# Performance work log

Measured on AMD Instinct MI355X. Metric: run time of the kernel, lower is better.

## Reference

```python
import jax, jax.numpy as jnp
import numpy as np

W0_SIREN = 30.0  # omega_0 used in sine activations

HID = [64, 64, 256, 256, 256]
IN_DIM = 65   # 64 feat channels + 1 time channel
OUT_DIM = 64


def _siren_params(key):
    dims = [IN_DIM] + HID + [OUT_DIM]
    params = []
    for i in range(len(dims) - 1):
        fan_in, fan_out = dims[i], dims[i + 1]
        key, kw, kb = jax.random.split(key, 3)
        if i == 0:
            bound = 1.0 / fan_in
        else:
            bound = np.sqrt(6.0 / fan_in) / W0_SIREN
        W = jax.random.uniform(kw, (fan_out, fan_in), jnp.float32, -bound, bound)
        b = jax.random.uniform(kb, (fan_out,), jnp.float32, -bound, bound)
        params.append((W, b))
    return params


def setup_inputs() -> dict:
    key = jax.random.key(0)
    k_feat, k_t, k_p = jax.random.split(key, 3)
    feat = jax.random.normal(k_feat, (2, 64, 192, 320), jnp.float32)
    times = jax.random.uniform(k_t, (3,), jnp.float32)
    params = _siren_params(k_p)
    inp = {"feat": feat, "times": times}
    for i, (W, b) in enumerate(params):
        inp[f"w{i}"] = W
        inp[f"b{i}"] = b
    return inp


def _gather_full_grid(feat):
    """Nearest grid_sample (align_corners=False) at pixel-center coords over the full grid.
    Returns [B, H*W, C]."""
    B, C, H, W = feat.shape
    # make_coord pixel centers in [-1, 1]
    ys = -1.0 + (2.0 * jnp.arange(H, dtype=jnp.float32) + 1.0) / H
    xs = -1.0 + (2.0 * jnp.arange(W, dtype=jnp.float32) + 1.0) / W
    gy, gx = jnp.meshgrid(ys, xs, indexing="ij")          # [H, W] each
    gy, gx = gy.reshape(-1), gx.reshape(-1)               # [qs]
    # grid_sample nearest, align_corners=False unnormalization
    iy = jnp.clip(jnp.round(((gy + 1.0) * H - 1.0) / 2.0).astype(jnp.int32), 0, H - 1)
    ix = jnp.clip(jnp.round(((gx + 1.0) * W - 1.0) / 2.0).astype(jnp.int32), 0, W - 1)
    q = feat[:, :, iy, ix]                                # [B, C, qs] gather
    return jnp.transpose(q, (0, 2, 1))                    # [B, qs, C]


def _siren_mlp(x, ws, bs):
    h = x
    n = len(ws)
    for i in range(n - 1):
        h = jnp.sin(W0_SIREN * (h @ ws[i].T + bs[i]))
    return h @ ws[n - 1].T + bs[n - 1]                    # outermost linear


def reference(feat, times, w0, b0, w1, b1, w2, b2, w3, b3, w4, b4, w5, b5):
    ws = [w0, w1, w2, w3, w4, w5]
    bs = [b0, b1, b2, b3, b4, b5]
    B, C, H, W = feat.shape
    qs = H * W
    q_feat = _gather_full_grid(feat)                      # [B, qs, 64]
    preds = []
    for c in range(3):  # Training==True branch: 3 time stamps
        t = times[c]
        pe = jnp.full((B, qs, 1), 1.0, feat.dtype) * t    # time channel
        enc = jnp.concatenate([q_feat, pe], axis=-1)      # [B, qs, 65]
        out = _siren_mlp(enc.reshape(B * qs, IN_DIM), ws, bs)  # [B*qs, 64]
        # F.fold with kernel_size=1 == reshape back to spatial map
        pred = out.reshape(B, qs, OUT_DIM).transpose(0, 2, 1).reshape(B, OUT_DIM, H, W)
        preds.append(pred)
    return jnp.stack(preds, axis=0)                       # [3, B, 64, H, W]
```

## Files before the change

### kernel.cpp

```cpp
#include <hip/hip_runtime.h>
#include <hip/hip_bf16.h>

typedef __bf16 bf16_t;
typedef bf16_t bf16x8 __attribute__((ext_vector_type(8)));
typedef float f32x4 __attribute__((ext_vector_type(4)));
typedef unsigned short u16;
typedef unsigned int u32;

static constexpr int kHW = 192 * 320;
static constexpr float kC = 4.77464829275686f;

__device__ __forceinline__ u16 f2bf(float f) {
  u32 u = __float_as_uint(f);
  return (u16)((u + 0x7FFFu + ((u >> 16) & 1u)) >> 16);
}

__device__ __forceinline__ u32 pack2(float a, float b) {
  __hip_bfloat162 h = __float22bfloat162_rn(make_float2(a, b));
  union { __hip_bfloat162 h2; u32 u; } cv;
  cv.h2 = h;
  return cv.u;
}

__device__ __forceinline__ void lds_barrier() {
  __asm__ volatile("s_waitcnt lgkmcnt(0)\n\ts_barrier" ::: "memory");
}

static constexpr int OFF_W0 = 0;
static constexpr int OFF_W1 = 4096;
static constexpr int OFF_W2 = 8192;
static constexpr int OFF_W3 = 24576;
static constexpr int OFF_W4 = 90112;
static constexpr int OFF_W5 = 155648;
static constexpr int W_TOTAL = 172032;
static constexpr int B_TOTAL = 1024;
static constexpr size_t FEAT_BYTE_OFF = 348160;
static constexpr size_t WS_NEED = FEAT_BYTE_OFF + (size_t)1920 * 8192;

__global__ void convert_weights(const float* __restrict__ w0, const float* __restrict__ w1,
                                const float* __restrict__ w2, const float* __restrict__ w3,
                                const float* __restrict__ w4, const float* __restrict__ w5,
                                const float* __restrict__ b0, const float* __restrict__ b1,
                                const float* __restrict__ b2, const float* __restrict__ b3,
                                const float* __restrict__ b4, const float* __restrict__ b5,
                                u16* __restrict__ wb, float* __restrict__ bws) {
  int i = blockIdx.x * 256 + threadIdx.x;
  if (i < W_TOTAL) {
    float v, s = kC;
    if (i < OFF_W1)      { int o = i >> 6, k = i & 63; v = w0[o * 65 + k]; }
    else if (i < OFF_W2) { v = w1[i - OFF_W1]; }
    else if (i < OFF_W3) { v = w2[i - OFF_W2]; }
    else if (i < OFF_W4) { v = w3[i - OFF_W3]; }
    else if (i < OFF_W5) { v = w4[i - OFF_W4]; }
    else                 { v = w5[i - OFF_W5]; s = 1.0f; }
    wb[i] = f2bf(v * s);
  } else {
    int j = i - W_TOTAL;
    float v;
    if (j < 64)       v = kC * b0[j];
    else if (j < 128) v = kC * w0[(j - 64) * 65 + 64];
    else if (j < 192) v = kC * b1[j - 128];
    else if (j < 448) v = kC * b2[j - 192];
    else if (j < 704) v = kC * b3[j - 448];
    else if (j < 960) v = kC * b4[j - 704];
    else              v = b5[j - 960];
    bws[j] = v;
  }
}

__global__ void convert_feat(const float* __restrict__ feat, u16* __restrict__ featT) {
  const int chunk = blockIdx.x;
  const int bq  = chunk / 960;
  const int hw0 = (chunk % 960) * 64;
  const int tid = threadIdx.x;
  const int p   = tid & 63;
  const int gg  = tid >> 6;
  const float* fbase = feat + (size_t)bq * 64 * kHW + hw0 + p;
  u16* img = featT + (size_t)chunk * 4096;
#pragma unroll
  for (int j = 0; j < 2; ++j) {
    const int g = gg * 2 + j;
    float v[8];
#pragma unroll
    for (int e = 0; e < 8; ++e) v[e] = fbase[(size_t)(g * 8 + e) * kHW];
    uint4 pk;
    pk.x = pack2(v[0], v[1]);
    pk.y = pack2(v[2], v[3]);
    pk.z = pack2(v[4], v[5]);
    pk.w = pack2(v[6], v[7]);
    *reinterpret_cast<uint4*>(img + p * 64 + ((g ^ (p & 7)) * 8)) = pk;
  }
}

template<int RSO>
__device__ __forceinline__ void epilogue_sin(f32x4 acc, u16* outb, int p, int g,
                                             int quad, int sw) {
  float s0 = __builtin_amdgcn_sinf(__builtin_amdgcn_fractf(acc[0]));
  float s1 = __builtin_amdgcn_sinf(__builtin_amdgcn_fractf(acc[1]));
  float s2 = __builtin_amdgcn_sinf(__builtin_amdgcn_fractf(acc[2]));
  float s3 = __builtin_amdgcn_sinf(__builtin_amdgcn_fractf(acc[3]));
  uint2 v;
  v.x = pack2(s0, s1);
  v.y = pack2(s2, s3);
  *reinterpret_cast<uint2*>(outb + p * RSO + ((g ^ sw) * 8) + (quad & 1) * 4) = v;
}

template<int NOT, int KT, int K>
__device__ __forceinline__ void load_wf(bf16x8 (&wf)[NOT][KT], const u16* __restrict__ wb,
                                        int wave, int l15, int quad) {
#pragma unroll
  for (int ks = 0; ks < KT; ++ks)
#pragma unroll
    for (int ot = 0; ot < NOT; ++ot)
      wf[ot][ks] = *reinterpret_cast<const bf16x8*>(
          wb + ((wave * NOT + ot) * 16 + l15) * K + ks * 32 + quad * 8);
}

template<int NOT>
__device__ __forceinline__ void load_bv(f32x4 (&bv)[NOT], const float* __restrict__ bg,
                                        int wave, int quad) {
#pragma unroll
  for (int ot = 0; ot < NOT; ++ot)
    bv[ot] = *reinterpret_cast<const f32x4*>(bg + (wave * NOT + ot) * 16 + quad * 4);
}

template<bool PRE>
__global__ void __launch_bounds__(256, 2)
siren_main(const float* __restrict__ feat, const float* __restrict__ times,
           const u16* __restrict__ wb, const float* __restrict__ bws,
           const u16* __restrict__ featT, float* __restrict__ out) {
  __shared__ __align__(16) u16 A32[64 * 256];
  __shared__ __align__(16) u16 B32[64 * 256];
  u16* X = B32;
  u16* Y = B32 + 4096;

  const int tid   = threadIdx.x;
  const int bid   = blockIdx.x;
  const int c     = bid / 1920;
  const int chunk = bid % 1920;
  const int bq    = chunk / 960;
  const int hw0   = (chunk % 960) * 64;
  const float t   = times[c];
  const int wave  = tid >> 6;
  const int lane  = tid & 63;
  const int l15   = lane & 15;
  const int quad  = lane >> 4;
  const int sw    = l15 & 7;

  bf16x8 wf0[1][2], wf1[1][2];
  load_wf<1, 2, 64>(wf0, wb + OFF_W0, wave, l15, quad);
  load_wf<1, 2, 64>(wf1, wb + OFF_W1, wave, l15, quad);
  f32x4 bv0;
  {
    f32x4 cb = *reinterpret_cast<const f32x4*>(bws + wave * 16 + quad * 4);
    f32x4 cw = *reinterpret_cast<const f32x4*>(bws + 64 + wave * 16 + quad * 4);
#pragma unroll
    for (int r = 0; r < 4; ++r) bv0[r] = cb[r] + t * cw[r];
  }
  f32x4 bv1 = *reinterpret_cast<const f32x4*>(bws + 128 + wave * 16 + quad * 4);

  if constexpr (PRE) {
    const uint4* src = reinterpret_cast<const uint4*>(featT + (size_t)chunk * 4096);
    uint4* dst = reinterpret_cast<uint4*>(X);
    dst[tid]       = src[tid];
    dst[tid + 256] = src[tid + 256];
  } else {
    const int p  = tid & 63;
    const int gg = tid >> 6;
    const float* fbase = feat + (size_t)bq * 64 * kHW + hw0 + p;
#pragma unroll
    for (int j = 0; j < 2; ++j) {
      const int g = gg * 2 + j;
      float v[8];
#pragma unroll
      for (int e = 0; e < 8; ++e) v[e] = fbase[(size_t)(g * 8 + e) * kHW];
      uint4 pk;
      pk.x = pack2(v[0], v[1]);
      pk.y = pack2(v[2], v[3]);
      pk.z = pack2(v[4], v[5]);
      pk.w = pack2(v[6], v[7]);
      *reinterpret_cast<uint4*>(X + p * 64 + ((g ^ (p & 7)) * 8)) = pk;
    }
  }
  lds_barrier();

  bf16x8 wf2[4][2];
  f32x4  bv2[4];
  {
    bf16x8 af[4][2];
#pragma unroll
    for (int pt = 0; pt < 4; ++pt)
#pragma unroll
      for (int ks = 0; ks < 2; ++ks)
        af[pt][ks] = *reinterpret_cast<const bf16x8*>(
            X + (pt * 16 + l15) * 64 + (((ks * 4 + quad) ^ sw) * 8));
    f32x4 acc[4];
#pragma unroll
    for (int pt = 0; pt < 4; ++pt) {
      acc[pt] = bv0;
      acc[pt] = __builtin_amdgcn_mfma_f32_16x16x32_bf16(wf0[0][0], af[pt][0], acc[pt], 0, 0, 0);
      acc[pt] = __builtin_amdgcn_mfma_f32_16x16x32_bf16(wf0[0][1], af[pt][1], acc[pt], 0, 0, 0);
    }
    load_wf<4, 2, 64>(wf2, wb + OFF_W2, wave, l15, quad);
    load_bv<4>(bv2, bws + 192, wave, quad);
#pragma unroll
    for (int pt = 0; pt < 4; ++pt)
      epilogue_sin<64>(acc[pt], Y, pt * 16 + l15, wave * 2 + (quad >> 1), quad, sw);
  }
  lds_barrier();

  {
    bf16x8 af[4][2];
#pragma unroll
    for (int pt = 0; pt < 4; ++pt)
#pragma unroll
      for (int ks = 0; ks < 2; ++ks)
        af[pt][ks] = *reinterpret_cast<const bf16x8*>(
            Y + (pt * 16 + l15) * 64 + (((ks * 4 + quad) ^ sw) * 8));
    f32x4 acc[4];
#pragma unroll
    for (int pt = 0; pt < 4; ++pt) {
      acc[pt] = bv1;
      acc[pt] = __builtin_amdgcn_mfma_f32_16x16x32_bf16(wf1[0][0], af[pt][0], acc[pt], 0, 0, 0);
      acc[pt] = __builtin_amdgcn_mfma_f32_16x16x32_bf16(wf1[0][1], af[pt][1], acc[pt], 0, 0, 0);
    }
#pragma unroll
    for (int pt = 0; pt < 4; ++pt)
      epilogue_sin<64>(acc[pt], X, pt * 16 + l15, wave * 2 + (quad >> 1), quad, sw);
  }
  lds_barrier();

  bf16x8 wf3[4][8];
  f32x4  bv3[4];
  {
    bf16x8 af[4][2];
#pragma unroll
    for (int pt = 0; pt < 4; ++pt)
#pragma unroll
      for (int ks = 0; ks < 2; ++ks)
        af[pt][ks] = *reinterpret_cast<const bf16x8*>(
            X + (pt * 16 + l15) * 64 + (((ks * 4 + quad) ^ sw) * 8));
    f32x4 acc[4][4];
#pragma unroll
    for (int pt = 0; pt < 4; ++pt)
#pragma unroll
      for (int ot = 0; ot < 4; ++ot) {
        acc[pt][ot] = bv2[ot];
        acc[pt][ot] = __builtin_amdgcn_mfma_f32_16x16x32_bf16(wf2[ot][0], af[pt][0], acc[pt][ot], 0, 0, 0);
        acc[pt][ot] = __builtin_amdgcn_mfma_f32_16x16x32_bf16(wf2[ot][1], af[pt][1], acc[pt][ot], 0, 0, 0);
      }
    load_wf<4, 8, 256>(wf3, wb + OFF_W3, wave, l15, quad);
    load_bv<4>(bv3, bws + 448, wave, quad);
#pragma unroll
    for (int pt = 0; pt < 4; ++pt)
#pragma unroll
      for (int ot = 0; ot < 4; ++ot)
        epilogue_sin<256>(acc[pt][ot], A32, pt * 16 + l15,
                          (wave * 4 + ot) * 2 + (quad >> 1), quad, sw);
  }
  lds_barrier();

  bf16x8 wf4[4][8];
  f32x4  bv4[4];
  {
#pragma unroll
    for (int pt = 0; pt < 4; ++pt) {
      bf16x8 af[8];
#pragma unroll
      for (int ks = 0; ks < 8; ++ks)
        af[ks] = *reinterpret_cast<const bf16x8*>(
            A32 + (pt * 16 + l15) * 256 + (((ks * 4 + quad) ^ sw) * 8));
      f32x4 acc[4];
#pragma unroll
      for (int ot = 0; ot < 4; ++ot) acc[ot] = bv3[ot];
#pragma unroll
      for (int ks = 0; ks < 8; ++ks)
#pragma unroll
        for (int ot = 0; ot < 4; ++ot)
          acc[ot] = __builtin_amdgcn_mfma_f32_16x16x32_bf16(wf3[ot][ks], af[ks], acc[ot], 0, 0, 0);
      if (pt == 3) {
        load_wf<4, 8, 256>(wf4, wb + OFF_W4, wave, l15, quad);
        load_bv<4>(bv4, bws + 704, wave, quad);
      }
#pragma unroll
      for (int ot = 0; ot < 4; ++ot)
        epilogue_sin<256>(acc[ot], B32, pt * 16 + l15,
                          (wave * 4 + ot) * 2 + (quad >> 1), quad, sw);
    }
  }
  lds_barrier();

  bf16x8 wf5[1][8];
  f32x4  bv5;
  {
#pragma unroll
    for (int pt = 0; pt < 4; ++pt) {
      bf16x8 af[8];
#pragma unroll
      for (int ks = 0; ks < 8; ++ks)
        af[ks] = *reinterpret_cast<const bf16x8*>(
            B32 + (pt * 16 + l15) * 256 + (((ks * 4 + quad) ^ sw) * 8));
      f32x4 acc[4];
#pragma unroll
      for (int ot = 0; ot < 4; ++ot) acc[ot] = bv4[ot];
#pragma unroll
      for (int ks = 0; ks < 8; ++ks)
#pragma unroll
        for (int ot = 0; ot < 4; ++ot)
          acc[ot] = __builtin_amdgcn_mfma_f32_16x16x32_bf16(wf4[ot][ks], af[ks], acc[ot], 0, 0, 0);
      if (pt == 3) {
        load_wf<1, 8, 256>(wf5, wb + OFF_W5, wave, l15, quad);
        bv5 = *reinterpret_cast<const f32x4*>(bws + 960 + wave * 16 + quad * 4);
      }
#pragma unroll
      for (int ot = 0; ot < 4; ++ot)
        epilogue_sin<256>(acc[ot], A32, pt * 16 + l15,
                          (wave * 4 + ot) * 2 + (quad >> 1), quad, sw);
    }
  }
  lds_barrier();

  {
    float* out_base = out + (size_t)(c * 2 + bq) * 64 * kHW + hw0;
#pragma unroll
    for (int pt = 0; pt < 4; ++pt) {
      bf16x8 af[8];
#pragma unroll
      for (int ks = 0; ks < 8; ++ks)
        af[ks] = *reinterpret_cast<const bf16x8*>(
            A32 + (pt * 16 + l15) * 256 + (((ks * 4 + quad) ^ sw) * 8));
      f32x4 acc = bv5;
#pragma unroll
      for (int ks = 0; ks < 8; ++ks)
        acc = __builtin_amdgcn_mfma_f32_16x16x32_bf16(wf5[0][ks], af[ks], acc, 0, 0, 0);
      const int p = pt * 16 + l15;
      const int o = wave * 16 + quad * 4;
      float* dst = out_base + (size_t)o * kHW + p;
#pragma unroll
      for (int r = 0; r < 4; ++r) dst[(size_t)r * kHW] = acc[r];
    }
  }
}

extern "C" void kernel_launch(void* const* d_in, const int* in_sizes, int n_in,
                              void* d_out, int out_size, void* d_ws, size_t ws_size,
                              hipStream_t stream) {
  const float* feat  = (const float*)d_in[0];
  const float* times = (const float*)d_in[1];
  const float* w0 = (const float*)d_in[2];
  const float* b0 = (const float*)d_in[3];
  const float* w1 = (const float*)d_in[4];
  const float* b1 = (const float*)d_in[5];
  const float* w2 = (const float*)d_in[6];
  const float* b2 = (const float*)d_in[7];
  const float* w3 = (const float*)d_in[8];
  const float* b3 = (const float*)d_in[9];
  const float* w4 = (const float*)d_in[10];
  const float* b4 = (const float*)d_in[11];
  const float* w5 = (const float*)d_in[12];
  const float* b5 = (const float*)d_in[13];
  u16*   wb  = (u16*)d_ws;
  float* bws = (float*)((char*)d_ws + (size_t)W_TOTAL * 2);
  float* out = (float*)d_out;

  convert_weights<<<(W_TOTAL + B_TOTAL) / 256, 256, 0, stream>>>(
      w0, w1, w2, w3, w4, w5, b0, b1, b2, b3, b4, b5, wb, bws);

  if (ws_size >= WS_NEED) {
    u16* featT = (u16*)((char*)d_ws + FEAT_BYTE_OFF);
    convert_feat<<<1920, 256, 0, stream>>>(feat, featT);
    siren_main<true><<<5760, 256, 0, stream>>>(feat, times, wb, bws, featT, out);
  } else {
    siren_main<false><<<5760, 256, 0, stream>>>(feat, times, wb, bws, wb, out);
  }
}
```

Baseline: 393.0 us.

## Software-pipeline LDS operand reads and split weight prefetch across layers

Restructures every layer so the LDS operand fragments for the next point tile are read while the current tile's MFMAs and sine epilogue run, using two double-buffered fragment sets. Weight prefetch for the 256-wide layers is split into two halves issued at different points to spread register pressure and global-load latency. In the PRE path, layer 0 now reads its operands directly from the pre-transposed global buffer, skipping the LDS staging copy and one barrier. The trade-off is higher register pressure; occupancy is pinned with waves_per_eu(2,2), which risks spills.

```diff
diff --git a/kernel.cpp b/kernel.cpp
--- a/kernel.cpp
+++ b/kernel.cpp
@@ -105,27 +105,13 @@
   *reinterpret_cast<uint2*>(outb + p * RSO + ((g ^ sw) * 8) + (quad & 1) * 4) = v;
 }
 
-template<int NOT, int KT, int K>
-__device__ __forceinline__ void load_wf(bf16x8 (&wf)[NOT][KT], const u16* __restrict__ wb,
-                                        int wave, int l15, int quad) {
-#pragma unroll
-  for (int ks = 0; ks < KT; ++ks)
-#pragma unroll
-    for (int ot = 0; ot < NOT; ++ot)
-      wf[ot][ks] = *reinterpret_cast<const bf16x8*>(
-          wb + ((wave * NOT + ot) * 16 + l15) * K + ks * 32 + quad * 8);
-}
-
-template<int NOT>
-__device__ __forceinline__ void load_bv(f32x4 (&bv)[NOT], const float* __restrict__ bg,
-                                        int wave, int quad) {
-#pragma unroll
-  for (int ot = 0; ot < NOT; ++ot)
-    bv[ot] = *reinterpret_cast<const f32x4*>(bg + (wave * NOT + ot) * 16 + quad * 4);
+__device__ __forceinline__ f32x4 mf(bf16x8 a, bf16x8 b, f32x4 c) {
+  return __builtin_amdgcn_mfma_f32_16x16x32_bf16(a, b, c, 0, 0, 0);
 }
 
 template<bool PRE>
-__global__ void __launch_bounds__(256, 2)
+__global__ __attribute__((amdgpu_waves_per_eu(2, 2)))
+void __launch_bounds__(256)
 siren_main(const float* __restrict__ feat, const float* __restrict__ times,
            const u16* __restrict__ wb, const float* __restrict__ bws,
            const u16* __restrict__ featT, float* __restrict__ out) {
@@ -147,192 +133,289 @@
   const int quad  = lane >> 4;
   const int sw    = l15 & 7;
 
-  bf16x8 wf0[1][2], wf1[1][2];
-  load_wf<1, 2, 64>(wf0, wb + OFF_W0, wave, l15, quad);
-  load_wf<1, 2, 64>(wf1, wb + OFF_W1, wave, l15, quad);
-  f32x4 bv0;
+  auto read_af8 = [&](bf16x8 (&af)[8], const u16* in, int pt) {
+#pragma unroll
+    for (int ks = 0; ks < 8; ++ks)
+      af[ks] = *reinterpret_cast<const bf16x8*>(
+          in + (pt * 16 + l15) * 256 + (((ks * 4 + quad) ^ sw) * 8));
+  };
+  auto read_af2 = [&](bf16x8 (&af)[2], const u16* in, int pt) {
+#pragma unroll
+    for (int ks = 0; ks < 2; ++ks)
+      af[ks] = *reinterpret_cast<const bf16x8*>(
+          in + (pt * 16 + l15) * 64 + (((ks * 4 + quad) ^ sw) * 8));
+  };
+  auto load_wf_half = [&](bf16x8 (&wf)[4][4], const u16* wbase, int kh) {
+#pragma unroll
+    for (int ks = 0; ks < 4; ++ks)
+#pragma unroll
+      for (int ot = 0; ot < 4; ++ot)
+        wf[ot][ks] = *reinterpret_cast<const bf16x8*>(
+            wbase + ((wave * 4 + ot) * 16 + l15) * 256 + (kh * 4 + ks) * 32 + quad * 8);
+  };
+  auto load_bv4 = [&](f32x4 (&bv)[4], const float* bg) {
+#pragma unroll
+    for (int ot = 0; ot < 4; ++ot)
+      bv[ot] = *reinterpret_cast<const f32x4*>(bg + (wave * 4 + ot) * 16 + quad * 4);
+  };
+  auto mfma_pt = [&](f32x4 (&acc)[4], bf16x8 (&wa)[4][4], bf16x8 (&wbh)[4][4],
+                     bf16x8 (&af)[8], const f32x4 (&bv)[4]) {
+#pragma unroll
+    for (int ot = 0; ot < 4; ++ot) acc[ot] = bv[ot];
+#pragma unroll
+    for (int ks = 0; ks < 8; ++ks)
+#pragma unroll
+      for (int ot = 0; ot < 4; ++ot)
+        acc[ot] = mf(ks < 4 ? wa[ot][ks] : wbh[ot][ks - 4], af[ks], acc[ot]);
+  };
+  auto epi_pt4 = [&](f32x4 (&acc)[4], u16* outb, int pt) {
+#pragma unroll
+    for (int ot = 0; ot < 4; ++ot)
+      epilogue_sin<256>(acc[ot], outb, pt * 16 + l15,
+                        (wave * 4 + ot) * 2 + (quad >> 1), quad, sw);
+  };
+
+  bf16x8 wf0[2], wf1[2];
+#pragma unroll
+  for (int ks = 0; ks < 2; ++ks) {
+    wf0[ks] = *reinterpret_cast<const bf16x8*>(wb + OFF_W0 + (wave * 16 + l15) * 64 + ks * 32 + quad * 8);
+    wf1[ks] = *reinterpret_cast<const bf16x8*>(wb + OFF_W1 + (wave * 16 + l15) * 64 + ks * 32 + quad * 8);
+  }
+  f32x4 bv0, bv1;
   {
     f32x4 cb = *reinterpret_cast<const f32x4*>(bws + wave * 16 + quad * 4);
     f32x4 cw = *reinterpret_cast<const f32x4*>(bws + 64 + wave * 16 + quad * 4);
 #pragma unroll
     for (int r = 0; r < 4; ++r) bv0[r] = cb[r] + t * cw[r];
-  }
-  f32x4 bv1 = *reinterpret_cast<const f32x4*>(bws + 128 + wave * 16 + quad * 4);
-
-  if constexpr (PRE) {
-    const uint4* src = reinterpret_cast<const uint4*>(featT + (size_t)chunk * 4096);
-    uint4* dst = reinterpret_cast<uint4*>(X);
-    dst[tid]       = src[tid];
-    dst[tid + 256] = src[tid + 256];
-  } else {
-    const int p  = tid & 63;
-    const int gg = tid >> 6;
-    const float* fbase = feat + (size_t)bq * 64 * kHW + hw0 + p;
-#pragma unroll
-    for (int j = 0; j < 2; ++j) {
-      const int g = gg * 2 + j;
-      float v[8];
-#pragma unroll
-      for (int e = 0; e < 8; ++e) v[e] = fbase[(size_t)(g * 8 + e) * kHW];
-      uint4 pk;
-      pk.x = pack2(v[0], v[1]);
-      pk.y = pack2(v[2], v[3]);
-      pk.z = pack2(v[4], v[5]);
-      pk.w = pack2(v[6], v[7]);
-      *reinterpret_cast<uint4*>(X + p * 64 + ((g ^ (p & 7)) * 8)) = pk;
-    }
-  }
-  lds_barrier();
+    bv1 = *reinterpret_cast<const f32x4*>(bws + 128 + wave * 16 + quad * 4);
+  }
 
   bf16x8 wf2[4][2];
   f32x4  bv2[4];
-  {
-    bf16x8 af[4][2];
-#pragma unroll
-    for (int pt = 0; pt < 4; ++pt)
+
+  if constexpr (PRE) {
+    const u16* fsrc = featT + (size_t)chunk * 4096;
+    bf16x8 a0[2], a1[2];
+    auto rdg = [&](bf16x8 (&a)[2], int pt) {
 #pragma unroll
       for (int ks = 0; ks < 2; ++ks)
-        af[pt][ks] = *reinterpret_cast<const bf16x8*>(
-            X + (pt * 16 + l15) * 64 + (((ks * 4 + quad) ^ sw) * 8));
-    f32x4 acc[4];
+        a[ks] = *reinterpret_cast<const bf16x8*>(
+            fsrc + (pt * 16 + l15) * 64 + (((ks * 4 + quad) ^ sw) * 8));
+    };
+    rdg(a0, 0);
+    rdg(a1, 1);
+#pragma unroll
+    for (int ks = 0; ks < 2; ++ks)
+#pragma unroll
+      for (int ot = 0; ot < 4; ++ot)
+        wf2[ot][ks] = *reinterpret_cast<const bf16x8*>(
+            wb + OFF_W2 + ((wave * 4 + ot) * 16 + l15) * 64 + ks * 32 + quad * 8);
+    load_bv4(bv2, bws + 192);
+
+    f32x4 acc;
+    acc = bv0; acc = mf(wf0[0], a0[0], acc); acc = mf(wf0[1], a0[1], acc);
+    rdg(a0, 2);
+    epilogue_sin<64>(acc, Y, 0 * 16 + l15, wave * 2 + (quad >> 1), quad, sw);
+    acc = bv0; acc = mf(wf0[0], a1[0], acc); acc = mf(wf0[1], a1[1], acc);
+    rdg(a1, 3);
+    epilogue_sin<64>(acc, Y, 1 * 16 + l15, wave * 2 + (quad >> 1), quad, sw);
+    acc = bv0; acc = mf(wf0[0], a0[0], acc); acc = mf(wf0[1], a0[1], acc);
+    epilogue_sin<64>(acc, Y, 2 * 16 + l15, wave * 2 + (quad >> 1), quad, sw);
+    acc = bv0; acc = mf(wf0[0], a1[0], acc); acc = mf(wf0[1], a1[1], acc);
+    epilogue_sin<64>(acc, Y, 3 * 16 + l15, wave * 2 + (quad >> 1), quad, sw);
+  } else {
+    {
+      const int p  = tid & 63;
+      const int gg = tid >> 6;
+      const float* fbase = feat + (size_t)bq * 64 * kHW + hw0 + p;
+#pragma unroll
+      for (int j = 0; j < 2; ++j) {
+        const int g = gg * 2 + j;
+        float v[8];
+#pragma unroll
+        for (int e = 0; e < 8; ++e) v[e] = fbase[(size_t)(g * 8 + e) * kHW];
+        uint4 pk;
+        pk.x = pack2(v[0], v[1]);
+        pk.y = pack2(v[2], v[3]);
+        pk.z = pack2(v[4], v[5]);
+        pk.w = pack2(v[6], v[7]);
+        *reinterpret_cast<uint4*>(X + p * 64 + ((g ^ (p & 7)) * 8)) = pk;
+      }
+    }
+    lds_barrier();
+#pragma unroll
+    for (int ks = 0; ks < 2; ++ks)
+#pragma unroll
+      for (int ot = 0; ot < 4; ++ot)
+        wf2[ot][ks] = *reinterpret_cast<const bf16x8*>(
+            wb + OFF_W2 + ((wave * 4 + ot) * 16 + l15) * 64 + ks * 32 + quad * 8);
+    load_bv4(bv2, bws + 192);
 #pragma unroll
     for (int pt = 0; pt < 4; ++pt) {
-      acc[pt] = bv0;
-      acc[pt] = __builtin_amdgcn_mfma_f32_16x16x32_bf16(wf0[0][0], af[pt][0], acc[pt], 0, 0, 0);
-      acc[pt] = __builtin_amdgcn_mfma_f32_16x16x32_bf16(wf0[0][1], af[pt][1], acc[pt], 0, 0, 0);
-    }
-    load_wf<4, 2, 64>(wf2, wb + OFF_W2, wave, l15, quad);
-    load_bv<4>(bv2, bws + 192, wave, quad);
-#pragma unroll
-    for (int pt = 0; pt < 4; ++pt)
-      epilogue_sin<64>(acc[pt], Y, pt * 16 + l15, wave * 2 + (quad >> 1), quad, sw);
+      bf16x8 a[2];
+      read_af2(a, X, pt);
+      f32x4 acc = bv0;
+      acc = mf(wf0[0], a[0], acc); acc = mf(wf0[1], a[1], acc);
+      epilogue_sin<64>(acc, Y, pt * 16 + l15, wave * 2 + (quad >> 1), quad, sw);
+    }
   }
   lds_barrier();
 
-  {
-    bf16x8 af[4][2];
-#pragma unroll
-    for (int pt = 0; pt < 4; ++pt)
-#pragma unroll
-      for (int ks = 0; ks < 2; ++ks)
-        af[pt][ks] = *reinterpret_cast<const bf16x8*>(
-            Y + (pt * 16 + l15) * 64 + (((ks * 4 + quad) ^ sw) * 8));
-    f32x4 acc[4];
+  bf16x8 wf3a[4][4], wf3b[4][4];
+  f32x4  bv3[4];
+  {
+    bf16x8 a0[2], a1[2];
+    read_af2(a0, Y, 0);
+    read_af2(a1, Y, 1);
+    load_wf_half(wf3a, wb + OFF_W3, 0);
+    load_bv4(bv3, bws + 448);
+    f32x4 acc;
+    acc = bv1; acc = mf(wf1[0], a0[0], acc); acc = mf(wf1[1], a0[1], acc);
+    read_af2(a0, Y, 2);
+    epilogue_sin<64>(acc, X, 0 * 16 + l15, wave * 2 + (quad >> 1), quad, sw);
+    acc = bv1; acc = mf(wf1[0], a1[0], acc); acc = mf(wf1[1], a1[1], acc);
+    read_af2(a1, Y, 3);
+    epilogue_sin<64>(acc, X, 1 * 16 + l15, wave * 2 + (quad >> 1), quad, sw);
+    acc = bv1; acc = mf(wf1[0], a0[0], acc); acc = mf(wf1[1], a0[1], acc);
+    epilogue_sin<64>(acc, X, 2 * 16 + l15, wave * 2 + (quad >> 1), quad, sw);
+    acc = bv1; acc = mf(wf1[0], a1[0], acc); acc = mf(wf1[1], a1[1], acc);
+    epilogue_sin<64>(acc, X, 3 * 16 + l15, wave * 2 + (quad >> 1), quad, sw);
+  }
+  lds_barrier();
+
+  {
+    bf16x8 a0[2], a1[2];
+    read_af2(a0, X, 0);
+    read_af2(a1, X, 1);
+    {
+      f32x4 acc[4];
+#pragma unroll
+      for (int ot = 0; ot < 4; ++ot) {
+        acc[ot] = bv2[ot];
+        acc[ot] = mf(wf2[ot][0], a0[0], acc[ot]);
+        acc[ot] = mf(wf2[ot][1], a0[1], acc[ot]);
+      }
+      read_af2(a0, X, 2);
+      epi_pt4(acc, A32, 0);
+    }
+    {
+      f32x4 acc[4];
+#pragma unroll
+      for (int ot = 0; ot < 4; ++ot) {
+        acc[ot] = bv2[ot];
+        acc[ot] = mf(wf2[ot][0], a1[0], acc[ot]);
+        acc[ot] = mf(wf2[ot][1], a1[1], acc[ot]);
+      }
+      read_af2(a1, X, 3);
+      epi_pt4(acc, A32, 1);
+    }
+    {
+      f32x4 acc[4];
+#pragma unroll
+      for (int ot = 0; ot < 4; ++ot) {
+        acc[ot] = bv2[ot];
+        acc[ot] = mf(wf2[ot][0], a0[0], acc[ot]);
+        acc[ot] = mf(wf2[ot][1], a0[1], acc[ot]);
+      }
+      load_wf_half(wf3b, wb + OFF_W3, 1);
+      epi_pt4(acc, A32, 2);
+    }
+    {
+      f32x4 acc[4];
+#pragma unroll
+      for (int ot = 0; ot < 4; ++ot) {
+        acc[ot] = bv2[ot];
+        acc[ot] = mf(wf2[ot][0], a1[0], acc[ot]);
+        acc[ot] = mf(wf2[ot][1], a1[1], acc[ot]);
+      }
+      epi_pt4(acc, A32, 3);
+    }
+  }
+  lds_barrier();
+
+  bf16x8 wf4a[4][4], wf4b[4][4];
+  f32x4  bv4[4];
+  {
+    bf16x8 afA[8], afB[8];
+    read_af8(afA, A32, 0);
+    read_af8(afB, A32, 1);
+    {
+      f32x4 acc[4];
+      mfma_pt(acc, wf3a, wf3b, afA, bv3);
+      read_af8(afA, A32, 2);
+      epi_pt4(acc, B32, 0);
+    }
+    {
+      f32x4 acc[4];
+      mfma_pt(acc, wf3a, wf3b, afB, bv3);
+      read_af8(afB, A32, 3);
+      epi_pt4(acc, B32, 1);
+    }
+    {
+      f32x4 acc[4];
+      mfma_pt(acc, wf3a, wf3b, afA, bv3);
+      epi_pt4(acc, B32, 2);
+    }
+    {
+      f32x4 acc[4];
+      mfma_pt(acc, wf3a, wf3b, afB, bv3);
+      load_wf_half(wf4a, wb + OFF_W4, 0);
+      load_bv4(bv4, bws + 704);
+      epi_pt4(acc, B32, 3);
+    }
+  }
+  lds_barrier();
+
+  bf16x8 wf5[8];
+  f32x4  bv5;
+  {
+    load_wf_half(wf4b, wb + OFF_W4, 1);
+    bf16x8 afA[8], afB[8];
+    read_af8(afA, B32, 0);
+    read_af8(afB, B32, 1);
+    {
+      f32x4 acc[4];
+      mfma_pt(acc, wf4a, wf4b, afA, bv4);
+      read_af8(afA, B32, 2);
+      epi_pt4(acc, A32, 0);
+    }
+    {
+      f32x4 acc[4];
+      mfma_pt(acc, wf4a, wf4b, afB, bv4);
+      read_af8(afB, B32, 3);
+      epi_pt4(acc, A32, 1);
+    }
+    {
+      f32x4 acc[4];
+      mfma_pt(acc, wf4a, wf4b, afA, bv4);
+      epi_pt4(acc, A32, 2);
+    }
+    {
+      f32x4 acc[4];
+      mfma_pt(acc, wf4a, wf4b, afB, bv4);
+#pragma unroll
+      for (int ks = 0; ks < 8; ++ks)
+        wf5[ks] = *reinterpret_cast<const bf16x8*>(
+            wb + OFF_W5 + (wave * 16 + l15) * 256 + ks * 32 + quad * 8);
+      bv5 = *reinterpret_cast<const f32x4*>(bws + 960 + wave * 16 + quad * 4);
+      epi_pt4(acc, A32, 3);
+    }
+  }
+  lds_barrier();
+
+  {
+    float* out_base = out + (size_t)(c * 2 + bq) * 64 * kHW + hw0;
+    bf16x8 afA[8], afB[8];
+    read_af8(afA, A32, 0);
+    read_af8(afB, A32, 1);
 #pragma unroll
     for (int pt = 0; pt < 4; ++pt) {
-      acc[pt] = bv1;
-      acc[pt] = __builtin_amdgcn_mfma_f32_16x16x32_bf16(wf1[0][0], af[pt][0], acc[pt], 0, 0, 0);
-      acc[pt] = __builtin_amdgcn_mfma_f32_16x16x32_bf16(wf1[0][1], af[pt][1], acc[pt], 0, 0, 0);
-    }
-#pragma unroll
-    for (int pt = 0; pt < 4; ++pt)
-      epilogue_sin<64>(acc[pt], X, pt * 16 + l15, wave * 2 + (quad >> 1), quad, sw);
-  }
-  lds_barrier();
-
-  bf16x8 wf3[4][8];
-  f32x4  bv3[4];
-  {
-    bf16x8 af[4][2];
-#pragma unroll
-    for (int pt = 0; pt < 4; ++pt)
-#pragma unroll
-      for (int ks = 0; ks < 2; ++ks)
-        af[pt][ks] = *reinterpret_cast<const bf16x8*>(
-            X + (pt * 16 + l15) * 64 + (((ks * 4 + quad) ^ sw) * 8));
-    f32x4 acc[4][4];
-#pragma unroll
-    for (int pt = 0; pt < 4; ++pt)
-#pragma unroll
-      for (int ot = 0; ot < 4; ++ot) {
-        acc[pt][ot] = bv2[ot];
-        acc[pt][ot] = __builtin_amdgcn_mfma_f32_16x16x32_bf16(wf2[ot][0], af[pt][0], acc[pt][ot], 0, 0, 0);
-        acc[pt][ot] = __builtin_amdgcn_mfma_f32_16x16x32_bf16(wf2[ot][1], af[pt][1], acc[pt][ot], 0, 0, 0);
-      }
-    load_wf<4, 8, 256>(wf3, wb + OFF_W3, wave, l15, quad);
-    load_bv<4>(bv3, bws + 448, wave, quad);
-#pragma unroll
-    for (int pt = 0; pt < 4; ++pt)
-#pragma unroll
-      for (int ot = 0; ot < 4; ++ot)
-        epilogue_sin<256>(acc[pt][ot], A32, pt * 16 + l15,
-                          (wave * 4 + ot) * 2 + (quad >> 1), quad, sw);
-  }
-  lds_barrier();
-
-  bf16x8 wf4[4][8];
-  f32x4  bv4[4];
-  {
-#pragma unroll
-    for (int pt = 0; pt < 4; ++pt) {
-      bf16x8 af[8];
-#pragma unroll
-      for (int ks = 0; ks < 8; ++ks)
-        af[ks] = *reinterpret_cast<const bf16x8*>(
-            A32 + (pt * 16 + l15) * 256 + (((ks * 4 + quad) ^ sw) * 8));
-      f32x4 acc[4];
-#pragma unroll
-      for (int ot = 0; ot < 4; ++ot) acc[ot] = bv3[ot];
-#pragma unroll
-      for (int ks = 0; ks < 8; ++ks)
-#pragma unroll
-        for (int ot = 0; ot < 4; ++ot)
-          acc[ot] = __builtin_amdgcn_mfma_f32_16x16x32_bf16(wf3[ot][ks], af[ks], acc[ot], 0, 0, 0);
-      if (pt == 3) {
-        load_wf<4, 8, 256>(wf4, wb + OFF_W4, wave, l15, quad);
-        load_bv<4>(bv4, bws + 704, wave, quad);
-      }
-#pragma unroll
-      for (int ot = 0; ot < 4; ++ot)
-        epilogue_sin<256>(acc[ot], B32, pt * 16 + l15,
-                          (wave * 4 + ot) * 2 + (quad >> 1), quad, sw);
-    }
-  }
-  lds_barrier();
-
-  bf16x8 wf5[1][8];
-  f32x4  bv5;
-  {
-#pragma unroll
-    for (int pt = 0; pt < 4; ++pt) {
-      bf16x8 af[8];
-#pragma unroll
-      for (int ks = 0; ks < 8; ++ks)
-        af[ks] = *reinterpret_cast<const bf16x8*>(
-            B32 + (pt * 16 + l15) * 256 + (((ks * 4 + quad) ^ sw) * 8));
-      f32x4 acc[4];
-#pragma unroll
-      for (int ot = 0; ot < 4; ++ot) acc[ot] = bv4[ot];
-#pragma unroll
-      for (int ks = 0; ks < 8; ++ks)
-#pragma unroll
-        for (int ot = 0; ot < 4; ++ot)
-          acc[ot] = __builtin_amdgcn_mfma_f32_16x16x32_bf16(wf4[ot][ks], af[ks], acc[ot], 0, 0, 0);
-      if (pt == 3) {
-        load_wf<1, 8, 256>(wf5, wb + OFF_W5, wave, l15, quad);
-        bv5 = *reinterpret_cast<const f32x4*>(bws + 960 + wave * 16 + quad * 4);
-      }
-#pragma unroll
-      for (int ot = 0; ot < 4; ++ot)
-        epilogue_sin<256>(acc[ot], A32, pt * 16 + l15,
-                          (wave * 4 + ot) * 2 + (quad >> 1), quad, sw);
-    }
-  }
-  lds_barrier();
-
-  {
-    float* out_base = out + (size_t)(c * 2 + bq) * 64 * kHW + hw0;
-#pragma unroll
-    for (int pt = 0; pt < 4; ++pt) {
-      bf16x8 af[8];
-#pragma unroll
-      for (int ks = 0; ks < 8; ++ks)
-        af[ks] = *reinterpret_cast<const bf16x8*>(
-            A32 + (pt * 16 + l15) * 256 + (((ks * 4 + quad) ^ sw) * 8));
+      bf16x8 (&af)[8] = (pt & 1) ? afB : afA;
       f32x4 acc = bv5;
 #pragma unroll
-      for (int ks = 0; ks < 8; ++ks)
-        acc = __builtin_amdgcn_mfma_f32_16x16x32_bf16(wf5[0][ks], af[ks], acc, 0, 0, 0);
+      for (int ks = 0; ks < 8; ++ks) acc = mf(wf5[ks], af[ks], acc);
+      if (pt == 0) read_af8(afA, A32, 2);
+      if (pt == 1) read_af8(afB, A32, 3);
       const int p = pt * 16 + l15;
       const int o = wave * 16 + quad * 4;
       float* dst = out_base + (size_t)o * kHW + p;
```

Result: no change. 390.5 us (-0.6%).
